# Kernel optimization log

Measured on AMD Instinct MI355X. Metric: run time of the kernel, lower is better.

Reference implementation:

```python
import jax, jax.numpy as jnp
import numpy as np
import math

D_MODEL = 1024
N_HEADS = 16
D_K = D_MODEL // N_HEADS
NB_FEATURES = max(1, math.ceil(math.log(D_MODEL)))  # 7
D_FF = 4096
BH = 4  # block_size_h
BW = 4  # block_size_w
EPS_LN = 1e-6


def gelu_approx(x):
    c = math.sqrt(2.0 / math.pi)
    return 0.5 * x * (1.0 + jnp.tanh(c * (x + 0.044715 * x * x * x)))


def layer_norm(x, alpha, bias):
    # torch .std() uses ddof=1 (unbiased)
    mean = x.mean(axis=-1, keepdims=True)
    std = jnp.std(x, axis=-1, ddof=1, keepdims=True)
    return alpha * (x - mean) / (std + EPS_LN) + bias


def causal_performer(q_in, k_in, v_in, wq, wk, wv, wo, omega):
    B, Sq, D = q_in.shape
    Sk = k_in.shape[1]
    q = (q_in @ wq.T).reshape(B, Sq, N_HEADS, D_K)
    k = (k_in @ wk.T).reshape(B, Sk, N_HEADS, D_K)
    v = (v_in @ wv.T).reshape(B, Sk, N_HEADS, D_K)
    # exp kernel feature map: exp(-0.5 * (x @ omega^T)^2)
    qp = jnp.exp(-0.5 * jnp.square(q @ omega.T))  # (B,Sq,H,nb)
    kp = jnp.exp(-0.5 * jnp.square(k @ omega.T))  # (B,Sk,H,nb)
    qp = qp / (qp.sum(-1, keepdims=True) + 1e-6)
    kp = kp / (kp.sum(-1, keepdims=True) + 1e-6)
    K_cum = jnp.cumsum(kp, axis=1)                               # (B,Sk,H,nb)
    KV_cum = jnp.cumsum(kp[..., None] * v[..., None, :], axis=1)  # (B,Sk,H,nb,dk)
    key_idx = jnp.clip((jnp.arange(Sq) // BH + 1) * BW - 1, None, Sk - 1)
    K_sel = K_cum[:, key_idx]    # (B,Sq,H,nb)
    KV_sel = KV_cum[:, key_idx]  # (B,Sq,H,nb,dk)
    num = jnp.einsum('bshn,bshnd->bshd', qp, KV_sel)
    den = jnp.einsum('bshn,bshn->bsh', qp, K_sel)[..., None]
    out = (num / (den + 1e-6)).reshape(B, Sq, D)
    return out @ wo.T


def setup_inputs() -> dict:
    key = jax.random.key(0)
    ks = jax.random.split(key, 24)
    s = 0.02
    p = {}
    p['x'] = jax.random.normal(ks[0], (2, 4096, D_MODEL), jnp.float32)
    p['lto'] = jax.random.normal(ks[1], (2, 4096, D_MODEL), jnp.float32)
    for i, nm in enumerate(['wq_s', 'wk_s', 'wv_s', 'wo_s']):
        p[nm] = jax.random.normal(ks[2 + i], (D_MODEL, D_MODEL), jnp.float32) * s
    for i, nm in enumerate(['wq_c', 'wk_c', 'wv_c', 'wo_c']):
        p[nm] = jax.random.normal(ks[6 + i], (D_MODEL, D_MODEL), jnp.float32) * s
    p['omega_s'] = jax.random.normal(ks[10], (NB_FEATURES, D_K), jnp.float32) / math.sqrt(D_K)
    p['omega_c'] = jax.random.normal(ks[11], (NB_FEATURES, D_K), jnp.float32) / math.sqrt(D_K)
    p['w1'] = jax.random.normal(ks[12], (D_FF, D_MODEL), jnp.float32) * s
    p['b1'] = jnp.zeros((D_FF,), jnp.float32)
    p['w2'] = jax.random.normal(ks[13], (D_MODEL, D_FF), jnp.float32) * s
    p['b2'] = jnp.zeros((D_MODEL,), jnp.float32)
    for i in range(3):
        p[f'ln{i}_a'] = jnp.ones((D_MODEL,), jnp.float32)
        p[f'ln{i}_b'] = jnp.zeros((D_MODEL,), jnp.float32)
    return p


def reference(x, lto, wq_s, wk_s, wv_s, wo_s, wq_c, wk_c, wv_c, wo_c,
              omega_s, omega_c, w1, b1, w2, b2,
              ln0_a, ln0_b, ln1_a, ln1_b, ln2_a, ln2_b):
    # residual 0: self-attention on x
    xn = layer_norm(x, ln0_a, ln0_b)
    x = x + causal_performer(xn, xn, xn, wq_s, wk_s, wv_s, wo_s, omega_s)
    # residual 1: cross-attention, queries = normed lto, keys/values = updated x
    ln = layer_norm(lto, ln1_a, ln1_b)
    lto = lto + causal_performer(ln, x, x, wq_c, wk_c, wv_c, wo_c, omega_c)
    # residual 2: feed-forward
    fn = layer_norm(lto, ln2_a, ln2_b)
    ff = gelu_approx(fn @ w1.T + b1) @ w2.T + b2
    return lto + ff
```

## Files before the change

kernel.cpp:

```cpp
#include <hip/hip_runtime.h>
#include <cstdint>
#include <cstddef>

typedef __bf16 bf16;
typedef __bf16 bf16x8 __attribute__((ext_vector_type(8)));
typedef __bf16 bf16x4 __attribute__((ext_vector_type(4)));
typedef float  f32x4  __attribute__((ext_vector_type(4)));

#define NB 7
static constexpr int Bq = 2, Sq = 4096, Dm = 1024, Dff = 4096;
static constexpr int Mrows = Bq * Sq;
static constexpr int NCH = Sq / 4;
static constexpr int CSW = 464;

template <int V> struct ic { static constexpr int value = V; };

__device__ __forceinline__ void gload16(const void* g, void* l) {
  __builtin_amdgcn_global_load_lds((__attribute__((address_space(1))) void*)g,
                                   (__attribute__((address_space(3))) void*)l,
                                   16, 0, 0);
}

template <int N> __device__ __forceinline__ void wait_vmcnt() {
  asm volatile("s_waitcnt vmcnt(%0)" :: "n"(N) : "memory");
}
__device__ __forceinline__ void wait_lgkm0() {
  asm volatile("s_waitcnt lgkmcnt(0)" ::: "memory");
}
__device__ __forceinline__ void SB() { __builtin_amdgcn_sched_barrier(0); }

__device__ __forceinline__ float gelu_f(float x) {
  const float c = 0.79788456080286535588f;
  float z = c * (x + 0.044715f * x * x * x);
  float t = 1.f - 2.f / (__expf(2.f * z) + 1.f);
  return 0.5f * x * (1.f + t);
}

struct CvtA {
  const float* s[10];
  bf16* d[10];
  int start[11];
};
__global__ __launch_bounds__(256) void cvt10(CvtA a) {
  const int i = blockIdx.x * 256 + threadIdx.x;
  int r = 0;
#pragma unroll
  for (int k = 1; k < 10; ++k) r += (i >= a.start[k]);
  const int o = i - a.start[r];
  f32x4 v = *(const f32x4*)&a.s[r][(size_t)o * 4];
  bf16x4 ov;
#pragma unroll
  for (int e = 0; e < 4; ++e) ov[e] = (bf16)v[e];
  *(bf16x4*)&a.d[r][(size_t)o * 4] = ov;
}

__global__ __launch_bounds__(256) void ln_kernel(const float* __restrict__ x,
                                                 const float* __restrict__ alpha,
                                                 const float* __restrict__ beta,
                                                 bf16* __restrict__ out) {
  const int row = blockIdx.x, tid = threadIdx.x;
  const float* xr = x + (size_t)row * Dm;
  f32x4 v = *(const f32x4*)&xr[tid * 4];
  float s  = v[0] + v[1] + v[2] + v[3];
  float s2 = v[0]*v[0] + v[1]*v[1] + v[2]*v[2] + v[3]*v[3];
#pragma unroll
  for (int o = 32; o > 0; o >>= 1) { s += __shfl_xor(s, o); s2 += __shfl_xor(s2, o); }
  __shared__ float red[8];
  const int wid = tid >> 6, lane = tid & 63;
  if (lane == 0) { red[wid] = s; red[wid + 4] = s2; }
  __syncthreads();
  s  = red[0] + red[1] + red[2] + red[3];
  s2 = red[4] + red[5] + red[6] + red[7];
  const float mean = s * (1.f / 1024.f);
  float var = (s2 - s * mean) * (1.f / 1023.f);
  var = fmaxf(var, 0.f);
  const float inv = 1.f / (sqrtf(var) + 1e-6f);
  f32x4 a4 = *(const f32x4*)&alpha[tid * 4];
  f32x4 b4 = *(const f32x4*)&beta[tid * 4];
  bf16x4 o4;
#pragma unroll
  for (int e = 0; e < 4; ++e) o4[e] = (bf16)(a4[e] * (v[e] - mean) * inv + b4[e]);
  *(bf16x4*)&out[(size_t)row * Dm + tid * 4] = o4;
}

template <int MODE>
__global__ __launch_bounds__(256, 2) void gemm128(
    const bf16* __restrict__ A, const bf16* __restrict__ Bw,
    int M, int N, int K,
    const float* __restrict__ bias, const float* __restrict__ res,
    float* __restrict__ outF, bf16* __restrict__ outB) {
  __shared__ __align__(16) char lds[65536];

  const int tid = threadIdx.x;
  const int lane = tid & 63, wid = tid >> 6;
  const int wm = wid >> 1, wn = wid & 1;

  const int nwg = gridDim.x;
  const int nc = N >> 7;
  const int nsc = nc >> 3;
  const int lin = (blockIdx.x & 7) * (nwg >> 3) + (blockIdx.x >> 3);
  const int s = lin >> 6, w = lin & 63;
  const int sr = s / nsc, sc = s - sr * nsc;
  const int bm = (sr * 8 + (w >> 3)) * 128;
  const int bn = (sc * 8 + (w & 7)) * 128;
  const int NT = K >> 6;

  const int srow = tid >> 3;
  const int scol = ((tid & 7) ^ (srow & 7)) * 8;
  const bf16* pSA = A  + (size_t)(bm + srow) * K + scol;
  const bf16* pSB = Bw + (size_t)(bn + srow) * K + scol;
  const size_t cK = (size_t)32 * K;
  const int stDa = wid * 1024;

  auto stage = [&](int buf, const bf16* sa, const bf16* sb) {
#pragma unroll
    for (int c = 0; c < 4; ++c) {
      gload16(sa + (size_t)c * cK, &lds[buf * 16384 + c * 4096 + stDa]);
      gload16(sb + (size_t)c * cK, &lds[32768 + buf * 16384 + c * 4096 + stDa]);
    }
  };

  const int lr = lane & 15, uo = lane >> 4;
  const int rdA0 = (wm * 64 + lr) * 128 + ((uo)     ^ (lr & 7)) * 16;
  const int rdA1 = (wm * 64 + lr) * 128 + ((4 + uo) ^ (lr & 7)) * 16;
  const int rdB0 = 32768 + (wn * 64 + lr) * 128 + ((uo)     ^ (lr & 7)) * 16;
  const int rdB1 = 32768 + (wn * 64 + lr) * 128 + ((4 + uo) ^ (lr & 7)) * 16;

  f32x4 acc[4][4] = {};
  bf16x8 a[4][2], b[4][2];

  stage(0, pSA, pSB);
  stage(1, pSA + 64, pSB + 64);
  pSA += 128; pSB += 128;
  wait_vmcnt<8>();
  __builtin_amdgcn_s_barrier();

  auto TILE = [&](auto BUFC, int tt) {
    constexpr int BUF = decltype(BUFC)::value;
#pragma unroll
    for (int i = 0; i < 4; ++i) {
      a[i][0] = *(const bf16x8*)&lds[rdA0 + BUF * 16384 + i * 2048];
      a[i][1] = *(const bf16x8*)&lds[rdA1 + BUF * 16384 + i * 2048];
    }
#pragma unroll
    for (int j = 0; j < 4; ++j) {
      b[j][0] = *(const bf16x8*)&lds[rdB0 + BUF * 16384 + j * 2048];
      b[j][1] = *(const bf16x8*)&lds[rdB1 + BUF * 16384 + j * 2048];
    }
    wait_lgkm0(); SB();
    __builtin_amdgcn_s_barrier(); SB();

    if (tt + 2 < NT) stage(BUF, pSA + (size_t)(tt & 1) * 64,
                                pSB + (size_t)(tt & 1) * 64);
    SB();
    __builtin_amdgcn_s_setprio(1);
#pragma unroll
    for (int i = 0; i < 4; ++i)
#pragma unroll
      for (int j = 0; j < 4; ++j) {
        acc[i][j] = __builtin_amdgcn_mfma_f32_16x16x32_bf16(a[i][0], b[j][0], acc[i][j], 0, 0, 0);
        acc[i][j] = __builtin_amdgcn_mfma_f32_16x16x32_bf16(a[i][1], b[j][1], acc[i][j], 0, 0, 0);
      }
    __builtin_amdgcn_s_setprio(0); SB();
    if (tt < NT - 2) wait_vmcnt<8>();
    else             wait_vmcnt<0>();
    __builtin_amdgcn_s_barrier(); SB();
  };

  for (int t = 0; t < NT; t += 2) {
    TILE(ic<0>{}, t);
    TILE(ic<1>{}, t + 1);
    pSA += 128; pSB += 128;
  }

#pragma unroll
  for (int f = 0; f < 4; ++f) {
    const int r0 = bm + wm * 64 + f * 16 + (lane >> 4) * 4;
#pragma unroll
    for (int g = 0; g < 4; ++g) {
      const int c = bn + wn * 64 + g * 16 + (lane & 15);
      float bv = 0.f;
      if (MODE == 3 || MODE == 4) bv = bias[c];
#pragma unroll
      for (int r = 0; r < 4; ++r) {
        const size_t idx = (size_t)(r0 + r) * N + c;
        float v = acc[f][g][r];
        if (MODE == 1 || MODE == 2) v += res[idx];
        if (MODE == 3) v = gelu_f(v + bv);
        if (MODE == 4) v += bv + res[idx];
        if (MODE == 0 || MODE == 1 || MODE == 3) outB[idx] = (bf16)v;
        else outF[idx] = v;
      }
    }
  }
}

__global__ __launch_bounds__(512) void perf_cs(
    const bf16* __restrict__ kmat, const bf16* __restrict__ vmat, int ld,
    const float* __restrict__ omega, float* __restrict__ CS,
    float* __restrict__ segtot) {
  const int tid = threadIdx.x;
  const int bh = blockIdx.y, b = bh >> 4, h = bh & 15;
  const int seg = blockIdx.x;
  const int s0 = seg * 512;
  __shared__ __align__(16) bf16 vs[512][64];
  __shared__ float kps[512][8];
  __shared__ float oms[448];

  {
    const bf16* vb = vmat + ((size_t)(b * Sq + s0)) * ld + h * 64;
#pragma unroll
    for (int p = 0; p < 8; ++p) {
      const int row = p * 64 + (tid >> 3), c16 = (tid & 7) * 8;
      *(uint4*)&vs[row][c16 ^ ((row & 7) * 8)] =
          *(const uint4*)&vb[(size_t)row * ld + c16];
    }
  }
  if (tid < 448) oms[tid] = omega[tid];
  __syncthreads();

  {
    const int row = tid;
    const bf16* kr = kmat + ((size_t)(b * Sq + s0 + row)) * ld + h * 64;
    bf16x8 kv[8];
#pragma unroll
    for (int q = 0; q < 8; ++q) kv[q] = *(const bf16x8*)&kr[q * 8];
    float f[NB];
#pragma unroll
    for (int n = 0; n < NB; ++n) f[n] = 0.f;
#pragma unroll
    for (int d = 0; d < 64; ++d) {
      const float kd = (float)kv[d >> 3][d & 7];
#pragma unroll
      for (int n = 0; n < NB; ++n) f[n] += kd * oms[n * 64 + d];
    }
    float sum = 1e-6f, e[NB];
#pragma unroll
    for (int n = 0; n < NB; ++n) { e[n] = __expf(-0.5f * f[n] * f[n]); sum += e[n]; }
    const float inv = 1.f / sum;
#pragma unroll
    for (int n = 0; n < NB; ++n) kps[row][n] = e[n] * inv;
    kps[row][7] = 0.f;
  }
  __syncthreads();

  if (tid < CSW) {
    const int comp = tid;
    float* outb = CS + ((size_t)bh * NCH + seg * 128) * CSW;
    float r = 0.f;
    if (comp < 8) {
      for (int c = 0; c < 128; ++c) {
        if (comp < 7)
          r += kps[4*c][comp] + kps[4*c+1][comp] + kps[4*c+2][comp] + kps[4*c+3][comp];
        outb[(size_t)c * CSW + comp] = r;
      }
    } else if (comp < 456) {
      const int n = (comp - 8) >> 6, d = (comp - 8) & 63;
      for (int c = 0; c < 128; ++c) {
#pragma unroll
        for (int i = 0; i < 4; ++i) {
          const int row = 4 * c + i;
          r += kps[row][n] * (float)vs[row][d ^ ((row & 7) * 8)];
        }
        outb[(size_t)c * CSW + comp] = r;
      }
    } else {
      for (int c = 0; c < 128; ++c) outb[(size_t)c * CSW + comp] = 0.f;
    }
    segtot[((size_t)bh * 8 + seg) * CSW + comp] = r;
  }
}

__global__ __launch_bounds__(256) void perf_scan2(float* __restrict__ segtot) {
  const int bh = blockIdx.x;
  const int c0 = threadIdx.x;
  float run0 = 0.f, run1 = 0.f;
#pragma unroll
  for (int s = 0; s < 8; ++s) {
    float* st = segtot + ((size_t)bh * 8 + s) * CSW;
    float t0 = st[c0]; st[c0] = run0; run0 += t0;
    if (c0 + 256 < CSW) { float t1 = st[c0 + 256]; st[c0 + 256] = run1; run1 += t1; }
  }
}

__global__ __launch_bounds__(256) void perf_out(
    const bf16* __restrict__ qmat, int ldq, const float* __restrict__ omega,
    const float* __restrict__ CS, const float* __restrict__ segtot,
    bf16* __restrict__ attn) {
  const int tid = threadIdx.x;
  const int bh = blockIdx.y, b = bh >> 4, h = bh & 15;
  const int s0 = blockIdx.x * 128;
  const int cg0 = s0 >> 2;
  const int seg = cg0 >> 7;
  __shared__ __align__(16) float Ps[32 * CSW];
  __shared__ float qps[128][8];
  __shared__ float oms[NB * 64];

  {
    const float* src = CS + ((size_t)bh * NCH + cg0) * CSW;
    const float* off = segtot + ((size_t)bh * 8 + seg) * CSW;
    for (int i = tid; i < 32 * CSW / 4; i += 256) {
      f32x4 a = *(const f32x4*)&src[i * 4];
      f32x4 o = *(const f32x4*)&off[(i % (CSW / 4)) * 4];
      a += o;
      *(f32x4*)&Ps[i * 4] = a;
    }
  }
  if (tid < 224) { oms[tid] = omega[tid]; oms[tid + 224] = omega[tid + 224]; }
  __syncthreads();
  {
    const int p = tid >> 1, half = tid & 1;
    const bf16* qr = qmat + ((size_t)(b * Sq + s0 + p)) * ldq + h * 64 + half * 32;
    bf16x8 qv[4];
#pragma unroll
    for (int q = 0; q < 4; ++q) qv[q] = *(const bf16x8*)&qr[q * 8];
    float f[NB];
#pragma unroll
    for (int n = 0; n < NB; ++n) f[n] = 0.f;
#pragma unroll
    for (int d = 0; d < 32; ++d) {
      float qd = (float)qv[d >> 3][d & 7];
#pragma unroll
      for (int n = 0; n < NB; ++n) f[n] += qd * oms[n * 64 + half * 32 + d];
    }
    float sum = 1e-6f;
    float e[NB];
#pragma unroll
    for (int n = 0; n < NB; ++n) {
      float full = f[n] + __shfl_xor(f[n], 1);
      e[n] = __expf(-0.5f * full * full);
      sum += e[n];
    }
    float inv = 1.f / sum;
    if (half == 0) {
      float den = 1e-6f;
      const float* Pr = &Ps[(p >> 2) * CSW];
#pragma unroll
      for (int n = 0; n < NB; ++n) {
        float qn = e[n] * inv;
        qps[p][n] = qn;
        den += qn * Pr[n];
      }
      qps[p][7] = 1.f / den;
    }
  }
  __syncthreads();
  {
    const int d = tid & 63, w = tid >> 6;
    for (int qq = w; qq < 128; qq += 4) {
      const float* Pr = &Ps[(qq >> 2) * CSW + 8 + d];
      float num = 0.f;
#pragma unroll
      for (int n = 0; n < NB; ++n) num += qps[qq][n] * Pr[n * 64];
      attn[((size_t)(b * Sq + s0 + qq)) * Dm + h * 64 + d] = (bf16)(num * qps[qq][7]);
    }
  }
}

extern "C" void kernel_launch(void* const* d_in, const int* in_sizes, int n_in,
                              void* d_out, int out_size, void* d_ws, size_t ws_size,
                              hipStream_t stream) {
  const float* x    = (const float*)d_in[0];
  const float* lto  = (const float*)d_in[1];
  const float* w_s[4] = {(const float*)d_in[2], (const float*)d_in[3],
                         (const float*)d_in[4], (const float*)d_in[5]};
  const float* w_c[4] = {(const float*)d_in[6], (const float*)d_in[7],
                         (const float*)d_in[8], (const float*)d_in[9]};
  const float* omega_s = (const float*)d_in[10];
  const float* omega_c = (const float*)d_in[11];
  const float* w1 = (const float*)d_in[12];
  const float* b1 = (const float*)d_in[13];
  const float* w2 = (const float*)d_in[14];
  const float* b2 = (const float*)d_in[15];
  const float* ln_a[3] = {(const float*)d_in[16], (const float*)d_in[18], (const float*)d_in[20]};
  const float* ln_b[3] = {(const float*)d_in[17], (const float*)d_in[19], (const float*)d_in[21]};

  char* ws = (char*)d_ws;
  size_t off = 0;
  auto alloc = [&](size_t bytes) -> char* {
    char* p = ws + off;
    off += (bytes + 255) & ~(size_t)255;
    return p;
  };

  const size_t actB = (size_t)Mrows * Dm * sizeof(bf16);
  const size_t MB32 = (size_t)Mrows * 2048 * sizeof(bf16);

  bf16* wqkv = (bf16*)alloc((size_t)3072 * 1024 * 2);
  bf16* wo_sb = (bf16*)alloc((size_t)1024 * 1024 * 2);
  bf16* wq_cb = (bf16*)alloc((size_t)1024 * 1024 * 2);
  bf16* wkv  = (bf16*)alloc((size_t)2048 * 1024 * 2);
  bf16* wo_cb = (bf16*)alloc((size_t)1024 * 1024 * 2);
  bf16* w1b = (bf16*)alloc((size_t)Dff * Dm * 2);
  bf16* w2b = (bf16*)alloc((size_t)Dff * Dm * 2);
  bf16* xnb  = (bf16*)alloc(actB);
  char* pool = alloc((size_t)Mrows * Dff * 2);
  bf16* qkvb = (bf16*)pool;
  bf16* kvb  = (bf16*)pool;
  bf16* qb   = (bf16*)(pool + MB32);
  bf16* hb   = (bf16*)pool;
  bf16* attnb= (bf16*)alloc(actB);
  bf16* x2b  = (bf16*)alloc(actB);
  bf16* ln1b = (bf16*)alloc(actB);
  float* lto2 = (float*)alloc((size_t)Mrows * Dm * 4);
  float* CSb  = (float*)alloc((size_t)32 * NCH * CSW * 4);
  float* stb  = (float*)alloc((size_t)32 * 8 * CSW * 4);
  bf16* fnb = xnb;

  {
    CvtA a;
    const float* srcs[10] = {w_s[0], w_s[1], w_s[2], w_s[3], w_c[0],
                             w_c[1], w_c[2], w_c[3], w1, w2};
    bf16* dsts[10] = {wqkv, wqkv + 1048576, wqkv + 2097152, wo_sb, wq_cb,
                      wkv, wkv + 1048576, wo_cb, w1b, w2b};
    const int SM = 262144, LG = 1048576;
    int st = 0;
    for (int i = 0; i < 10; ++i) {
      a.s[i] = srcs[i]; a.d[i] = dsts[i]; a.start[i] = st;
      st += (i < 8) ? SM : LG;
    }
    a.start[10] = st;
    cvt10<<<st / 256, 256, 0, stream>>>(a);
  }

  dim3 gperf(Sq / 128, Bq * 16);
  dim3 gseg(8, Bq * 16);
  const int gQKV = (Mrows / 128) * (3072 / 128);
  const int gKV  = (Mrows / 128) * (2048 / 128);
  const int gFF1 = (Mrows / 128) * (4096 / 128);
  const int gN1k = (Mrows / 128) * (1024 / 128);

  ln_kernel<<<Mrows, 256, 0, stream>>>(x, ln_a[0], ln_b[0], xnb);
  gemm128<0><<<gQKV, 256, 0, stream>>>(xnb, wqkv, Mrows, 3072, 1024, nullptr, nullptr, nullptr, qkvb);
  perf_cs<<<gseg, 512, 0, stream>>>(qkvb + 1024, qkvb + 2048, 3072, omega_s, CSb, stb);
  perf_scan2<<<32, 256, 0, stream>>>(stb);
  perf_out<<<gperf, 256, 0, stream>>>(qkvb, 3072, omega_s, CSb, stb, attnb);
  gemm128<1><<<gN1k, 256, 0, stream>>>(attnb, wo_sb, Mrows, 1024, 1024, nullptr, x, nullptr, x2b);

  ln_kernel<<<Mrows, 256, 0, stream>>>(lto, ln_a[1], ln_b[1], ln1b);
  gemm128<0><<<gN1k, 256, 0, stream>>>(ln1b, wq_cb, Mrows, 1024, 1024, nullptr, nullptr, nullptr, qb);
  gemm128<0><<<gKV, 256, 0, stream>>>(x2b, wkv, Mrows, 2048, 1024, nullptr, nullptr, nullptr, kvb);
  perf_cs<<<gseg, 512, 0, stream>>>(kvb, kvb + 1024, 2048, omega_c, CSb, stb);
  perf_scan2<<<32, 256, 0, stream>>>(stb);
  perf_out<<<gperf, 256, 0, stream>>>(qb, 1024, omega_c, CSb, stb, attnb);
  gemm128<2><<<gN1k, 256, 0, stream>>>(attnb, wo_cb, Mrows, 1024, 1024, nullptr, lto, lto2, nullptr);

  ln_kernel<<<Mrows, 256, 0, stream>>>(lto2, ln_a[2], ln_b[2], fnb);
  gemm128<3><<<gFF1, 256, 0, stream>>>(fnb, w1b, Mrows, 4096, 1024, b1, nullptr, nullptr, hb);
  gemm128<4><<<gN1k, 256, 0, stream>>>(hb, w2b, Mrows, 1024, 4096, b2, lto2, (float*)d_out, nullptr);
}
```

Baseline: 511.1 us.

## Store performer prefix sums in bf16 and fold segment scan into output kernel

```diff
diff --git a/kernel.cpp b/kernel.cpp
--- a/kernel.cpp
+++ b/kernel.cpp
@@ -152,8 +152,6 @@
 
     if (tt + 2 < NT) stage(BUF, pSA + (size_t)(tt & 1) * 64,
                                 pSB + (size_t)(tt & 1) * 64);
-    SB();
-    __builtin_amdgcn_s_setprio(1);
 #pragma unroll
     for (int i = 0; i < 4; ++i)
 #pragma unroll
@@ -161,7 +159,7 @@
         acc[i][j] = __builtin_amdgcn_mfma_f32_16x16x32_bf16(a[i][0], b[j][0], acc[i][j], 0, 0, 0);
         acc[i][j] = __builtin_amdgcn_mfma_f32_16x16x32_bf16(a[i][1], b[j][1], acc[i][j], 0, 0, 0);
       }
-    __builtin_amdgcn_s_setprio(0); SB();
+    SB();
     if (tt < NT - 2) wait_vmcnt<8>();
     else             wait_vmcnt<0>();
     __builtin_amdgcn_s_barrier(); SB();
@@ -197,7 +195,7 @@
 
 __global__ __launch_bounds__(512) void perf_cs(
     const bf16* __restrict__ kmat, const bf16* __restrict__ vmat, int ld,
-    const float* __restrict__ omega, float* __restrict__ CS,
+    const float* __restrict__ omega, bf16* __restrict__ CS,
     float* __restrict__ segtot) {
   const int tid = threadIdx.x;
   const int bh = blockIdx.y, b = bh >> 4, h = bh & 15;
@@ -246,13 +244,13 @@
 
   if (tid < CSW) {
     const int comp = tid;
-    float* outb = CS + ((size_t)bh * NCH + seg * 128) * CSW;
+    bf16* outb = CS + ((size_t)bh * NCH + seg * 128) * CSW;
     float r = 0.f;
     if (comp < 8) {
       for (int c = 0; c < 128; ++c) {
         if (comp < 7)
           r += kps[4*c][comp] + kps[4*c+1][comp] + kps[4*c+2][comp] + kps[4*c+3][comp];
-        outb[(size_t)c * CSW + comp] = r;
+        outb[(size_t)c * CSW + comp] = (bf16)r;
       }
     } else if (comp < 456) {
       const int n = (comp - 8) >> 6, d = (comp - 8) & 63;
@@ -262,30 +260,18 @@
           const int row = 4 * c + i;
           r += kps[row][n] * (float)vs[row][d ^ ((row & 7) * 8)];
         }
-        outb[(size_t)c * CSW + comp] = r;
+        outb[(size_t)c * CSW + comp] = (bf16)r;
       }
     } else {
-      for (int c = 0; c < 128; ++c) outb[(size_t)c * CSW + comp] = 0.f;
+      for (int c = 0; c < 128; ++c) outb[(size_t)c * CSW + comp] = (bf16)0.f;
     }
     segtot[((size_t)bh * 8 + seg) * CSW + comp] = r;
-  }
-}
-
-__global__ __launch_bounds__(256) void perf_scan2(float* __restrict__ segtot) {
-  const int bh = blockIdx.x;
-  const int c0 = threadIdx.x;
-  float run0 = 0.f, run1 = 0.f;
-#pragma unroll
-  for (int s = 0; s < 8; ++s) {
-    float* st = segtot + ((size_t)bh * 8 + s) * CSW;
-    float t0 = st[c0]; st[c0] = run0; run0 += t0;
-    if (c0 + 256 < CSW) { float t1 = st[c0 + 256]; st[c0 + 256] = run1; run1 += t1; }
   }
 }
 
 __global__ __launch_bounds__(256) void perf_out(
     const bf16* __restrict__ qmat, int ldq, const float* __restrict__ omega,
-    const float* __restrict__ CS, const float* __restrict__ segtot,
+    const bf16* __restrict__ CS, const float* __restrict__ segtot,
     bf16* __restrict__ attn) {
   const int tid = threadIdx.x;
   const int bh = blockIdx.y, b = bh >> 4, h = bh & 15;
@@ -295,18 +281,27 @@
   __shared__ __align__(16) float Ps[32 * CSW];
   __shared__ float qps[128][8];
   __shared__ float oms[NB * 64];
-
-  {
-    const float* src = CS + ((size_t)bh * NCH + cg0) * CSW;
-    const float* off = segtot + ((size_t)bh * 8 + seg) * CSW;
+  __shared__ float offs[CSW];
+
+  for (int c = tid; c < CSW; c += 256) {
+    float o = 0.f;
+    for (int ss = 0; ss < seg; ++ss) o += segtot[((size_t)bh * 8 + ss) * CSW + c];
+    offs[c] = o;
+  }
+  if (tid < 224) { oms[tid] = omega[tid]; oms[tid + 224] = omega[tid + 224]; }
+  __syncthreads();
+
+  {
+    const bf16* src = CS + ((size_t)bh * NCH + cg0) * CSW;
     for (int i = tid; i < 32 * CSW / 4; i += 256) {
-      f32x4 a = *(const f32x4*)&src[i * 4];
-      f32x4 o = *(const f32x4*)&off[(i % (CSW / 4)) * 4];
-      a += o;
-      *(f32x4*)&Ps[i * 4] = a;
-    }
-  }
-  if (tid < 224) { oms[tid] = omega[tid]; oms[tid + 224] = omega[tid + 224]; }
+      bf16x4 a4 = *(const bf16x4*)&src[(size_t)i * 4];
+      const int c0 = (i % (CSW / 4)) * 4;
+      f32x4 o;
+#pragma unroll
+      for (int e = 0; e < 4; ++e) o[e] = (float)a4[e] + offs[c0 + e];
+      *(f32x4*)&Ps[i * 4] = o;
+    }
+  }
   __syncthreads();
   {
     const int p = tid >> 1, half = tid & 1;
@@ -403,7 +398,7 @@
   bf16* x2b  = (bf16*)alloc(actB);
   bf16* ln1b = (bf16*)alloc(actB);
   float* lto2 = (float*)alloc((size_t)Mrows * Dm * 4);
-  float* CSb  = (float*)alloc((size_t)32 * NCH * CSW * 4);
+  bf16*  CSb  = (bf16*)alloc((size_t)32 * NCH * CSW * 2);
   float* stb  = (float*)alloc((size_t)32 * 8 * CSW * 4);
   bf16* fnb = xnb;
 
@@ -433,7 +428,6 @@
   ln_kernel<<<Mrows, 256, 0, stream>>>(x, ln_a[0], ln_b[0], xnb);
   gemm128<0><<<gQKV, 256, 0, stream>>>(xnb, wqkv, Mrows, 3072, 1024, nullptr, nullptr, nullptr, qkvb);
   perf_cs<<<gseg, 512, 0, stream>>>(qkvb + 1024, qkvb + 2048, 3072, omega_s, CSb, stb);
-  perf_scan2<<<32, 256, 0, stream>>>(stb);
   perf_out<<<gperf, 256, 0, stream>>>(qkvb, 3072, omega_s, CSb, stb, attnb);
   gemm128<1><<<gN1k, 256, 0, stream>>>(attnb, wo_sb, Mrows, 1024, 1024, nullptr, x, nullptr, x2b);
 
@@ -441,7 +435,6 @@
   gemm128<0><<<gN1k, 256, 0, stream>>>(ln1b, wq_cb, Mrows, 1024, 1024, nullptr, nullptr, nullptr, qb);
   gemm128<0><<<gKV, 256, 0, stream>>>(x2b, wkv, Mrows, 2048, 1024, nullptr, nullptr, nullptr, kvb);
   perf_cs<<<gseg, 512, 0, stream>>>(kvb, kvb + 1024, 2048, omega_c, CSb, stb);
-  perf_scan2<<<32, 256, 0, stream>>>(stb);
   perf_out<<<gperf, 256, 0, stream>>>(qb, 1024, omega_c, CSb, stb, attnb);
   gemm128<2><<<gN1k, 256, 0, stream>>>(attnb, wo_cb, Mrows, 1024, 1024, nullptr, lto, lto2, nullptr);
 
```

Result: faster. 500.0 us (median of 2 runs) (-2.2%).
